# Kernel optimization log

Measured on AMD Instinct MI355X. Metric: run time of the kernel, lower is better.

Reference implementation:

```python
import jax, jax.numpy as jnp
import numpy as np

N = 50000      # nodes
E = 800000     # edges (avg degree 16)
DIN = 64       # input feature dim
DOUT = 64      # output feature dim
NSLOPE = 0.2   # LeakyReLU negative slope


def setup_inputs() -> dict:
    key = jax.random.key(0)
    k1, k2, k3, k4 = jax.random.split(key, 4)
    x = jax.random.normal(k1, (N, DIN), dtype=jnp.float32)
    W = jax.random.normal(k2, (DOUT, DIN), dtype=jnp.float32) * (1.0 / np.sqrt(DIN))
    b = jnp.zeros((DOUT,), dtype=jnp.float32)
    a = jax.random.normal(k3, (DOUT,), dtype=jnp.float32) * (1.0 / np.sqrt(DOUT))
    edge_index = jax.random.randint(k4, (2, E), 0, N, dtype=jnp.int32)
    return {"x": x, "W": W, "b": b, "a": a, "edge_index": edge_index}


def reference(x, W, b, a, edge_index):
    # GATv2: e_ij = a^T LeakyReLU(W h_i + W h_j + b); softmax over incoming
    # neighbors j of node i; h_i' = sigmoid(sum_j alpha_ij * W h_j)
    Wh = x @ W.T + b                          # [N, DOUT]
    src, dst = edge_index[0], edge_index[1]   # edge j -> i
    s = Wh[dst] + Wh[src]                     # [E, DOUT] per-edge pre-activation
    e = jnp.where(s > 0, s, NSLOPE * s) @ a   # [E] attention logits
    # numerically stable segment softmax over destination nodes
    emax = jax.ops.segment_max(e, dst, num_segments=N)       # [N]
    emax = jnp.where(jnp.isfinite(emax), emax, 0.0)          # nodes with no edges
    ex = jnp.exp(e - emax[dst])                               # [E]
    denom = jax.ops.segment_sum(ex, dst, num_segments=N)      # [N]
    alpha = ex / jnp.maximum(denom[dst], 1e-9)                # [E]
    agg = jax.ops.segment_sum(alpha[:, None] * Wh[src], dst, num_segments=N)
    return jax.nn.sigmoid(agg)                # [N, DOUT]
```

## Files before the change

kernel.cpp:

```cpp
#include <hip/hip_runtime.h>
#include <hip/hip_bf16.h>
#include <math.h>

#define NN 50000
#define EE 800000
#define DD 64
#define NSLOPE 0.2f
#define NBUCK 196
#define CAP 4608
#define CHUNK 4096
#define BINB 196
#define WHB 1024
#define WHWAVES (WHB * 4)

__device__ __forceinline__ float leaky(float s) { return s > 0.f ? s : NSLOPE * s; }

__global__ void __launch_bounds__(256) bin_kernel(
    const int* __restrict__ ei, unsigned int* __restrict__ gbuf,
    int* __restrict__ gCursor) {
    __shared__ int cnt[256];
    __shared__ int excl[256];
    __shared__ int cur[256];
    __shared__ int base[256];
    __shared__ unsigned int pairs[CHUNK];
    int tid = threadIdx.x;
    int start = blockIdx.x * CHUNK;
    int nedge = min(CHUNK, EE - start);
    cnt[tid] = 0; cur[tid] = 0;
    __syncthreads();
    for (int j = 0; j < CHUNK / 256; ++j) {
        int i = start + tid + j * 256;
        if (i < EE) {
            unsigned int dst = (unsigned int)ei[EE + i];
            atomicAdd(&cnt[dst >> 8], 1);
        }
    }
    __syncthreads();
    int v = cnt[tid];
    excl[tid] = v; __syncthreads();
    for (int o = 1; o < 256; o <<= 1) {
        int t = (tid >= o) ? excl[tid - o] : 0;
        __syncthreads();
        excl[tid] += t;
        __syncthreads();
    }
    int ex = excl[tid] - v;
    __syncthreads();
    excl[tid] = ex;
    __syncthreads();
    for (int j = 0; j < CHUNK / 256; ++j) {
        int i = start + tid + j * 256;
        if (i < EE) {
            unsigned int src = (unsigned int)ei[i];
            unsigned int dst = (unsigned int)ei[EE + i];
            int b = dst >> 8;
            int r = atomicAdd(&cur[b], 1);
            pairs[excl[b] + r] = (dst << 16) | src;
        }
    }
    if (tid < NBUCK) base[tid] = atomicAdd(&gCursor[tid], cnt[tid]);
    __syncthreads();
    for (int i = tid; i < nedge; i += 256) {
        unsigned int p = pairs[i];
        int b = p >> 24;
        gbuf[(size_t)b * CAP + base[b] + (i - excl[b])] = p;
    }
}

__global__ void __launch_bounds__(256) bucketscan_kernel(
    const int* __restrict__ gCursor, int* __restrict__ bucketBase,
    int* __restrict__ off) {
    __shared__ int s[256];
    int tid = threadIdx.x;
    int v = (tid < NBUCK) ? gCursor[tid] : 0;
    s[tid] = v; __syncthreads();
    for (int o = 1; o < 256; o <<= 1) {
        int t = (tid >= o) ? s[tid - o] : 0;
        __syncthreads();
        s[tid] += t;
        __syncthreads();
    }
    if (tid <= NBUCK) bucketBase[tid] = s[tid] - v;
    if (tid == 0) off[NN] = EE;
}

__global__ void __launch_bounds__(256) csr_wh_kernel(
    const unsigned int* __restrict__ gbuf, const int* __restrict__ gCursor,
    const int* __restrict__ bucketBase, int* __restrict__ off,
    unsigned short* __restrict__ csr,
    const float* __restrict__ x, const float* __restrict__ W,
    const float* __restrict__ bias, float* __restrict__ Wh) {
    __shared__ int hist[256];
    __shared__ int excl[256];
    __shared__ int cur[256];
    __shared__ float4 Wl[DD * 16];
    __shared__ float xrow[4][DD];
    int tid = threadIdx.x;

    if (blockIdx.x < NBUCK) {
        int k = blockIdx.x;
        int cnt = gCursor[k];
        int base_k = bucketBase[k];
        const unsigned int* bp = gbuf + (size_t)k * CAP;
        hist[tid] = 0; cur[tid] = 0;
        __syncthreads();
        for (int i = tid; i < cnt; i += 256)
            atomicAdd(&hist[(bp[i] >> 16) & 255], 1);
        __syncthreads();
        int v = hist[tid];
        excl[tid] = v; __syncthreads();
        for (int o = 1; o < 256; o <<= 1) {
            int t = (tid >= o) ? excl[tid - o] : 0;
            __syncthreads();
            excl[tid] += t;
            __syncthreads();
        }
        int ex = excl[tid] - v;
        __syncthreads();
        excl[tid] = ex;
        __syncthreads();
        int dst = k * 256 + tid;
        if (dst < NN) off[dst] = base_k + ex;
        for (int i = tid; i < cnt; i += 256) {
            unsigned int p = bp[i];
            int local = (p >> 16) & 255;
            int slot = base_k + excl[local] + atomicAdd(&cur[local], 1);
            csr[slot] = (unsigned short)(p & 0xffffu);
        }
        return;
    }

    int bid = blockIdx.x - NBUCK;
    const float4* W4 = (const float4*)W;
    for (int i = tid; i < DD * 16; i += 256) {
        int c = i >> 4, k4 = i & 15;
        Wl[c * 16 + (k4 ^ (c & 15))] = W4[i];
    }
    __syncthreads();
    int wv = tid >> 6, c = tid & 63;
    float4 wc[16];
#pragma unroll
    for (int k4 = 0; k4 < 16; ++k4) wc[k4] = Wl[c * 16 + (k4 ^ (c & 15))];
    float bv = bias[c];
    int row = bid * 4 + wv;
    float xv = x[(size_t)row * DD + c];
    while (row < NN) {
        xrow[wv][c] = xv;
        int nrow = row + WHWAVES;
        if (nrow < NN) xv = x[(size_t)nrow * DD + c];
        float acc = bv;
#pragma unroll
        for (int k4 = 0; k4 < 16; ++k4) {
            float4 q = *(const float4*)&xrow[wv][k4 * 4];
            acc += wc[k4].x * q.x + wc[k4].y * q.y + wc[k4].z * q.z + wc[k4].w * q.w;
        }
        Wh[(size_t)row * DD + c] = acc;
        row = nrow;
    }
}

__global__ void __launch_bounds__(256) fused_kernel(
    const float4* __restrict__ Wh4, const float4* __restrict__ a4,
    const int* __restrict__ off, const unsigned short* __restrict__ csr,
    float4* __restrict__ out4) {
    int wave = threadIdx.x >> 6, lane = threadIdx.x & 63;
    int node = blockIdx.x * 4 + wave;
    int b = lane >> 4, f4 = lane & 15;
    float4 av  = a4[f4];
    float4 whi = Wh4[(size_t)node * 16 + f4];
    int beg = off[node], end = off[node + 1];
    float den = 0.f;
    float4 acc = make_float4(0.f, 0.f, 0.f, 0.f);
    float4 whs_n = make_float4(0.f, 0.f, 0.f, 0.f);
    if (beg < end) {
        int i0 = beg + b;
        int s0 = csr[(i0 < end) ? i0 : (end - 1)];
        whs_n = Wh4[(size_t)s0 * 16 + f4];
    }
    for (int base = beg; base < end; base += 4) {
        float4 whs = whs_n;
        int ni = base + 4 + b;
        if (ni < end) {
            int s2 = csr[ni];
            whs_n = Wh4[(size_t)s2 * 16 + f4];
        }
        float t = av.x * leaky(whi.x + whs.x) + av.y * leaky(whi.y + whs.y)
                + av.z * leaky(whi.z + whs.z) + av.w * leaky(whi.w + whs.w);
        t += __shfl_xor(t, 1, 64);
        t += __shfl_xor(t, 2, 64);
        t += __shfl_xor(t, 4, 64);
        t += __shfl_xor(t, 8, 64);
        float ex = (base + b < end) ? __expf(t) : 0.f;
        den += ex;
        acc.x += ex * whs.x; acc.y += ex * whs.y;
        acc.z += ex * whs.z; acc.w += ex * whs.w;
    }
    acc.x += __shfl_xor(acc.x, 16, 64); acc.y += __shfl_xor(acc.y, 16, 64);
    acc.z += __shfl_xor(acc.z, 16, 64); acc.w += __shfl_xor(acc.w, 16, 64);
    den   += __shfl_xor(den,   16, 64);
    acc.x += __shfl_xor(acc.x, 32, 64); acc.y += __shfl_xor(acc.y, 32, 64);
    acc.z += __shfl_xor(acc.z, 32, 64); acc.w += __shfl_xor(acc.w, 32, 64);
    den   += __shfl_xor(den,   32, 64);
    if (b == 0) {
        float id = 1.f / fmaxf(den, 1e-9f);
        float4 o;
        o.x = 1.f / (1.f + __expf(-acc.x * id));
        o.y = 1.f / (1.f + __expf(-acc.y * id));
        o.z = 1.f / (1.f + __expf(-acc.z * id));
        o.w = 1.f / (1.f + __expf(-acc.w * id));
        out4[(size_t)node * 16 + f4] = o;
    }
}

extern "C" void kernel_launch(void* const* d_in, const int* in_sizes, int n_in,
                              void* d_out, int out_size, void* d_ws, size_t ws_size,
                              hipStream_t stream) {
    const float* x = (const float*)d_in[0];
    const float* W = (const float*)d_in[1];
    const float* b = (const float*)d_in[2];
    const float* a = (const float*)d_in[3];
    const int*   ei = (const int*)d_in[4];
    float* out = (float*)d_out;

    char* ws = (char*)d_ws;
    float*          Wh         = (float*)(ws);
    int*            gCursor    = (int*)(ws + 12800000);
    int*            bucketBase = (int*)(ws + 12801024);
    int*            off        = (int*)(ws + 12802048);
    unsigned int*   gbuf       = (unsigned int*)(ws + 13002112);
    unsigned short* csr        = (unsigned short*)(ws + 16614784);

    hipMemsetAsync(gCursor, 0, 1024, stream);
    bin_kernel<<<BINB, 256, 0, stream>>>(ei, gbuf, gCursor);
    bucketscan_kernel<<<1, 256, 0, stream>>>(gCursor, bucketBase, off);
    csr_wh_kernel<<<NBUCK + WHB, 256, 0, stream>>>(gbuf, gCursor, bucketBase, off,
                                                   csr, x, W, b, Wh);
    fused_kernel<<<NN / 4, 256, 0, stream>>>((const float4*)Wh, (const float4*)a,
                                             off, csr, (float4*)out);
}
```

Baseline: 144.2 us.

## Merge bucket scan into CSR kernel and co-schedule Wh GEMM with binning

Drops the single-block bucketscan kernel by having every CSR block recompute the prefix sum over bucket counts. The Wh projection moves into the binning launch, so it runs alongside edge binning instead of alongside CSR construction. The GEMM is also rewritten to stage a 64-row x tile in shared memory and compute 16 rows per thread with register accumulators. This removes one launch and one serialization point and raises reuse of the W registers, but each CSR block now repeats a redundant 196-entry scan.

```diff
diff --git a/kernel.cpp b/kernel.cpp
--- a/kernel.cpp
+++ b/kernel.cpp
@@ -10,104 +10,34 @@
 #define CAP 4608
 #define CHUNK 4096
 #define BINB 196
-#define WHB 1024
-#define WHWAVES (WHB * 4)
+#define WHB 782
 
 __device__ __forceinline__ float leaky(float s) { return s > 0.f ? s : NSLOPE * s; }
 
-__global__ void __launch_bounds__(256) bin_kernel(
+__global__ void __launch_bounds__(256) bin_wh_kernel(
     const int* __restrict__ ei, unsigned int* __restrict__ gbuf,
-    int* __restrict__ gCursor) {
-    __shared__ int cnt[256];
-    __shared__ int excl[256];
-    __shared__ int cur[256];
-    __shared__ int base[256];
-    __shared__ unsigned int pairs[CHUNK];
-    int tid = threadIdx.x;
-    int start = blockIdx.x * CHUNK;
-    int nedge = min(CHUNK, EE - start);
-    cnt[tid] = 0; cur[tid] = 0;
-    __syncthreads();
-    for (int j = 0; j < CHUNK / 256; ++j) {
-        int i = start + tid + j * 256;
-        if (i < EE) {
-            unsigned int dst = (unsigned int)ei[EE + i];
-            atomicAdd(&cnt[dst >> 8], 1);
-        }
-    }
-    __syncthreads();
-    int v = cnt[tid];
-    excl[tid] = v; __syncthreads();
-    for (int o = 1; o < 256; o <<= 1) {
-        int t = (tid >= o) ? excl[tid - o] : 0;
-        __syncthreads();
-        excl[tid] += t;
-        __syncthreads();
-    }
-    int ex = excl[tid] - v;
-    __syncthreads();
-    excl[tid] = ex;
-    __syncthreads();
-    for (int j = 0; j < CHUNK / 256; ++j) {
-        int i = start + tid + j * 256;
-        if (i < EE) {
-            unsigned int src = (unsigned int)ei[i];
-            unsigned int dst = (unsigned int)ei[EE + i];
-            int b = dst >> 8;
-            int r = atomicAdd(&cur[b], 1);
-            pairs[excl[b] + r] = (dst << 16) | src;
-        }
-    }
-    if (tid < NBUCK) base[tid] = atomicAdd(&gCursor[tid], cnt[tid]);
-    __syncthreads();
-    for (int i = tid; i < nedge; i += 256) {
-        unsigned int p = pairs[i];
-        int b = p >> 24;
-        gbuf[(size_t)b * CAP + base[b] + (i - excl[b])] = p;
-    }
-}
-
-__global__ void __launch_bounds__(256) bucketscan_kernel(
-    const int* __restrict__ gCursor, int* __restrict__ bucketBase,
-    int* __restrict__ off) {
-    __shared__ int s[256];
-    int tid = threadIdx.x;
-    int v = (tid < NBUCK) ? gCursor[tid] : 0;
-    s[tid] = v; __syncthreads();
-    for (int o = 1; o < 256; o <<= 1) {
-        int t = (tid >= o) ? s[tid - o] : 0;
-        __syncthreads();
-        s[tid] += t;
-        __syncthreads();
-    }
-    if (tid <= NBUCK) bucketBase[tid] = s[tid] - v;
-    if (tid == 0) off[NN] = EE;
-}
-
-__global__ void __launch_bounds__(256) csr_wh_kernel(
-    const unsigned int* __restrict__ gbuf, const int* __restrict__ gCursor,
-    const int* __restrict__ bucketBase, int* __restrict__ off,
-    unsigned short* __restrict__ csr,
+    int* __restrict__ gCursor,
     const float* __restrict__ x, const float* __restrict__ W,
     const float* __restrict__ bias, float* __restrict__ Wh) {
-    __shared__ int hist[256];
-    __shared__ int excl[256];
-    __shared__ int cur[256];
-    __shared__ float4 Wl[DD * 16];
-    __shared__ float xrow[4][DD];
+    __shared__ __align__(16) char smem[32768];
     int tid = threadIdx.x;
 
-    if (blockIdx.x < NBUCK) {
-        int k = blockIdx.x;
-        int cnt = gCursor[k];
-        int base_k = bucketBase[k];
-        const unsigned int* bp = gbuf + (size_t)k * CAP;
-        hist[tid] = 0; cur[tid] = 0;
-        __syncthreads();
-        for (int i = tid; i < cnt; i += 256)
-            atomicAdd(&hist[(bp[i] >> 16) & 255], 1);
-        __syncthreads();
-        int v = hist[tid];
+    if (blockIdx.x < BINB) {
+        int* cnt  = (int*)smem;
+        int* excl = cnt + 256;
+        int* cur  = cnt + 512;
+        int* base = cnt + 768;
+        unsigned int* pairs = (unsigned int*)(smem + 4096);
+        int start = blockIdx.x * CHUNK;
+        int nedge = min(CHUNK, EE - start);
+        cnt[tid] = 0; cur[tid] = 0;
+        __syncthreads();
+        for (int j = 0; j < CHUNK / 256; ++j) {
+            int i = start + tid + j * 256;
+            if (i < EE) atomicAdd(&cnt[((unsigned int)ei[EE + i]) >> 8], 1);
+        }
+        __syncthreads();
+        int v = cnt[tid];
         excl[tid] = v; __syncthreads();
         for (int o = 1; o < 256; o <<= 1) {
             int t = (tid >= o) ? excl[tid - o] : 0;
@@ -119,43 +49,111 @@
         __syncthreads();
         excl[tid] = ex;
         __syncthreads();
-        int dst = k * 256 + tid;
-        if (dst < NN) off[dst] = base_k + ex;
-        for (int i = tid; i < cnt; i += 256) {
-            unsigned int p = bp[i];
-            int local = (p >> 16) & 255;
-            int slot = base_k + excl[local] + atomicAdd(&cur[local], 1);
-            csr[slot] = (unsigned short)(p & 0xffffu);
+        for (int j = 0; j < CHUNK / 256; ++j) {
+            int i = start + tid + j * 256;
+            if (i < EE) {
+                unsigned int src = (unsigned int)ei[i];
+                unsigned int dst = (unsigned int)ei[EE + i];
+                int b = dst >> 8;
+                int r = atomicAdd(&cur[b], 1);
+                pairs[excl[b] + r] = (dst << 16) | src;
+            }
+        }
+        if (tid < NBUCK) base[tid] = atomicAdd(&gCursor[tid], cnt[tid]);
+        __syncthreads();
+        for (int i = tid; i < nedge; i += 256) {
+            unsigned int p = pairs[i];
+            int b = p >> 24;
+            gbuf[(size_t)b * CAP + base[b] + (i - excl[b])] = p;
         }
         return;
     }
 
-    int bid = blockIdx.x - NBUCK;
+    int bid = blockIdx.x - BINB;
+    float4* Wl = (float4*)smem;
+    float4* xt = (float4*)(smem + 16384);
     const float4* W4 = (const float4*)W;
-    for (int i = tid; i < DD * 16; i += 256) {
+    const float4* x4 = (const float4*)x;
+    for (int i = tid; i < 1024; i += 256) {
         int c = i >> 4, k4 = i & 15;
         Wl[c * 16 + (k4 ^ (c & 15))] = W4[i];
     }
-    __syncthreads();
-    int wv = tid >> 6, c = tid & 63;
-    float4 wc[16];
-#pragma unroll
-    for (int k4 = 0; k4 < 16; ++k4) wc[k4] = Wl[c * 16 + (k4 ^ (c & 15))];
+    int tilebase = bid * 1024;
+    for (int i = tid; i < 1024; i += 256) {
+        int gi = tilebase + i;
+        xt[i] = (gi < NN * 16) ? x4[gi] : make_float4(0.f, 0.f, 0.f, 0.f);
+    }
+    __syncthreads();
+    int r4 = tid >> 6, c = tid & 63;
+    float4 wreg[16];
+#pragma unroll
+    for (int k4 = 0; k4 < 16; ++k4) wreg[k4] = Wl[c * 16 + (k4 ^ (c & 15))];
     float bv = bias[c];
-    int row = bid * 4 + wv;
-    float xv = x[(size_t)row * DD + c];
-    while (row < NN) {
-        xrow[wv][c] = xv;
-        int nrow = row + WHWAVES;
-        if (nrow < NN) xv = x[(size_t)nrow * DD + c];
-        float acc = bv;
-#pragma unroll
-        for (int k4 = 0; k4 < 16; ++k4) {
-            float4 q = *(const float4*)&xrow[wv][k4 * 4];
-            acc += wc[k4].x * q.x + wc[k4].y * q.y + wc[k4].z * q.z + wc[k4].w * q.w;
-        }
-        Wh[(size_t)row * DD + c] = acc;
-        row = nrow;
+    float acc[16];
+#pragma unroll
+    for (int rr = 0; rr < 16; ++rr) acc[rr] = bv;
+#pragma unroll
+    for (int k4 = 0; k4 < 16; ++k4) {
+        float4 w = wreg[k4];
+#pragma unroll
+        for (int rr = 0; rr < 16; ++rr) {
+            float4 q = xt[(r4 * 16 + rr) * 16 + k4];
+            acc[rr] += w.x * q.x + w.y * q.y + w.z * q.z + w.w * q.w;
+        }
+    }
+    int row0 = bid * 64 + r4 * 16;
+#pragma unroll
+    for (int rr = 0; rr < 16; ++rr) {
+        int row = row0 + rr;
+        if (row < NN) Wh[(size_t)row * DD + c] = acc[rr];
+    }
+}
+
+__global__ void __launch_bounds__(256) csr_kernel(
+    const unsigned int* __restrict__ gbuf, const int* __restrict__ gCursor,
+    int* __restrict__ off, unsigned short* __restrict__ csr) {
+    __shared__ int s[256];
+    __shared__ int hist[256];
+    __shared__ int excl[256];
+    __shared__ int cur[256];
+    int tid = threadIdx.x;
+    int k = blockIdx.x;
+    int v = (tid < NBUCK) ? gCursor[tid] : 0;
+    s[tid] = v; __syncthreads();
+    for (int o = 1; o < 256; o <<= 1) {
+        int t = (tid >= o) ? s[tid - o] : 0;
+        __syncthreads();
+        s[tid] += t;
+        __syncthreads();
+    }
+    int base_k = (k == 0) ? 0 : s[k - 1];
+    int cnt = s[k] - base_k;
+    const unsigned int* bp = gbuf + (size_t)k * CAP;
+    hist[tid] = 0; cur[tid] = 0;
+    __syncthreads();
+    for (int i = tid; i < cnt; i += 256)
+        atomicAdd(&hist[(bp[i] >> 16) & 255], 1);
+    __syncthreads();
+    int hv = hist[tid];
+    excl[tid] = hv; __syncthreads();
+    for (int o = 1; o < 256; o <<= 1) {
+        int t = (tid >= o) ? excl[tid - o] : 0;
+        __syncthreads();
+        excl[tid] += t;
+        __syncthreads();
+    }
+    int hex = excl[tid] - hv;
+    __syncthreads();
+    excl[tid] = hex;
+    __syncthreads();
+    int dst = k * 256 + tid;
+    if (dst < NN) off[dst] = base_k + hex;
+    if (k == 0 && tid == 0) off[NN] = EE;
+    for (int i = tid; i < cnt; i += 256) {
+        unsigned int p = bp[i];
+        int local = (p >> 16) & 255;
+        int slot = base_k + excl[local] + atomicAdd(&cur[local], 1);
+        csr[slot] = (unsigned short)(p & 0xffffu);
     }
 }
 
@@ -223,18 +221,15 @@
     float* out = (float*)d_out;
 
     char* ws = (char*)d_ws;
-    float*          Wh         = (float*)(ws);
-    int*            gCursor    = (int*)(ws + 12800000);
-    int*            bucketBase = (int*)(ws + 12801024);
-    int*            off        = (int*)(ws + 12802048);
-    unsigned int*   gbuf       = (unsigned int*)(ws + 13002112);
-    unsigned short* csr        = (unsigned short*)(ws + 16614784);
+    float*          Wh      = (float*)(ws);
+    int*            gCursor = (int*)(ws + 12800000);
+    int*            off     = (int*)(ws + 12801024);
+    unsigned int*   gbuf    = (unsigned int*)(ws + 13001216);
+    unsigned short* csr     = (unsigned short*)(ws + 16613888);
 
     hipMemsetAsync(gCursor, 0, 1024, stream);
-    bin_kernel<<<BINB, 256, 0, stream>>>(ei, gbuf, gCursor);
-    bucketscan_kernel<<<1, 256, 0, stream>>>(gCursor, bucketBase, off);
-    csr_wh_kernel<<<NBUCK + WHB, 256, 0, stream>>>(gbuf, gCursor, bucketBase, off,
-                                                   csr, x, W, b, Wh);
+    bin_wh_kernel<<<BINB + WHB, 256, 0, stream>>>(ei, gbuf, gCursor, x, W, b, Wh);
+    csr_kernel<<<NBUCK, 256, 0, stream>>>(gbuf, gCursor, off, csr);
     fused_kernel<<<NN / 4, 256, 0, stream>>>((const float4*)Wh, (const float4*)a,
                                              off, csr, (float4*)out);
 }
```

Measured after the change: 380.5 us. +163.8%, slower.
